# Performance work log

Measured on AMD Instinct MI355X. Metric: run time of the kernel, lower is better.

## Reference

```python
import jax, jax.numpy as jnp
import numpy as np

N_NODES = 200000
N_GRAPHS = 4000


def _sage_conv(x, src, dst, W_l, b_l, W_r, num_nodes):
    # PyG SAGEConv (aggr='mean'): out = lin_l(mean_{j in N(i)} x_j) + lin_r(x_i)
    msg_sum = jax.ops.segment_sum(x[src], dst, num_segments=num_nodes)      # [N, d]
    deg = jax.ops.segment_sum(jnp.ones_like(src, dtype=x.dtype), dst,
                              num_segments=num_nodes)                       # [N]
    mean_nbr = msg_sum / jnp.maximum(deg, 1.0)[:, None]
    return mean_nbr @ W_l.T + b_l + x @ W_r.T


def setup_inputs() -> dict:
    key = jax.random.key(0)
    ks = jax.random.split(key, 10)
    in_ch, hid, out = 32, 64, 2
    E = 3200000
    x = jax.random.normal(ks[0], (N_NODES, in_ch), dtype=jnp.float32)
    edge_index = jax.random.randint(ks[1], (2, E), 0, N_NODES, dtype=jnp.int64)
    batch = jnp.sort(jax.random.randint(ks[2], (N_NODES,), 0, N_GRAPHS, dtype=jnp.int64))

    def glorot(k, shape):
        lim = 1.0 / np.sqrt(shape[1])
        return jax.random.uniform(k, shape, jnp.float32, -lim, lim)

    return {
        "x": x,
        "edge_index": edge_index,
        "batch": batch,
        "W1_l": glorot(ks[3], (hid, in_ch)),
        "b1": jnp.zeros((hid,), jnp.float32),
        "W1_r": glorot(ks[4], (hid, in_ch)),
        "W2_l": glorot(ks[5], (hid, hid)),
        "b2": jnp.zeros((hid,), jnp.float32),
        "W2_r": glorot(ks[6], (hid, hid)),
        "W_lin": glorot(ks[7], (out, hid)),
        "b_lin": jnp.zeros((out,), jnp.float32),
    }


def reference(x, edge_index, batch, W1_l, b1, W1_r, W2_l, b2, W2_r, W_lin, b_lin):
    src, dst = edge_index[0], edge_index[1]
    h = jax.nn.relu(_sage_conv(x, src, dst, W1_l, b1, W1_r, N_NODES))
    h = jax.nn.relu(_sage_conv(h, src, dst, W2_l, b2, W2_r, N_NODES))
    # global_mean_pool over graph ids
    pool_sum = jax.ops.segment_sum(h, batch, num_segments=N_GRAPHS)          # [G, 64]
    cnt = jax.ops.segment_sum(jnp.ones_like(batch, dtype=h.dtype), batch,
                              num_segments=N_GRAPHS)                          # [G]
    pooled = pool_sum / jnp.maximum(cnt, 1.0)[:, None]
    return pooled @ W_lin.T + b_lin
```

## Files before the change

kernel.cpp:

```cpp
#include <hip/hip_runtime.h>
#include <hip/hip_bf16.h>


#define WS_ALIGN 64
#define EPB 4096
#define BSHIFT 8
#define BNODES 256
#define BCAP 6144
#define MAXNB 1024

typedef short bf16x8 __attribute__((ext_vector_type(8)));
typedef float f32x4 __attribute__((ext_vector_type(4)));

__device__ inline unsigned short f2bf(float f) {
    unsigned u = __float_as_uint(f);
    return (unsigned short)((u + 0x7fffu + ((u >> 16) & 1u)) >> 16);
}

__device__ inline void acc8(const uint4 u, float* a) {
    a[0] += __uint_as_float(u.x << 16);
    a[1] += __uint_as_float(u.x & 0xffff0000u);
    a[2] += __uint_as_float(u.y << 16);
    a[3] += __uint_as_float(u.y & 0xffff0000u);
    a[4] += __uint_as_float(u.z << 16);
    a[5] += __uint_as_float(u.z & 0xffff0000u);
    a[6] += __uint_as_float(u.w << 16);
    a[7] += __uint_as_float(u.w & 0xffff0000u);
}


__global__ void prep_kernel(const float* __restrict__ x, unsigned short* __restrict__ xb,
                            const float* __restrict__ W1_l, const float* __restrict__ W1_r,
                            const float* __restrict__ W2_l, const float* __restrict__ W2_r,
                            unsigned short* __restrict__ whi1, unsigned short* __restrict__ whi2,
                            int* __restrict__ bucketCursor, float* __restrict__ pool,
                            int N, int NB, int G, int total4) {
    const int gid = blockIdx.x * blockDim.x + threadIdx.x;
    if (gid < total4) {
        const float4 v = reinterpret_cast<const float4*>(x)[gid];
        ushort4 o;
        o.x = f2bf(v.x); o.y = f2bf(v.y); o.z = f2bf(v.z); o.w = f2bf(v.w);
        reinterpret_cast<ushort4*>(xb)[gid] = o;
    }
    if (gid < NB) bucketCursor[gid] = gid * BCAP;
    if (gid < G * 64) pool[gid] = 0.0f;
    if (gid < 64 * 64) {
        const int o = gid >> 6, k = gid & 63;
        const float v = (k < 32) ? W1_l[o * 32 + k] : W1_r[o * 32 + (k - 32)];
        whi1[gid] = f2bf(v);
    }
    if (gid < 64 * 128) {
        const int o = gid >> 7, k = gid & 127;
        const float v = (k < 64) ? W2_l[o * 64 + k] : W2_r[o * 64 + (k - 64)];
        whi2[gid] = f2bf(v);
    }
}


__global__ __launch_bounds__(256) void bucket_scatter_kernel(const int* __restrict__ src,
                                                             const int* __restrict__ dst,
                                                             int* __restrict__ bucketCursor,
                                                             unsigned* __restrict__ bucketData,
                                                             int E, int NB) {
    __shared__ int hist[MAXNB];
    __shared__ int cur[MAXNB];
    const int t = threadIdx.x;
    for (int i = t; i < MAXNB; i += 256) hist[i] = 0;
    __syncthreads();
    const int eBase = blockIdx.x * EPB + t;
    int s[16], b[16], dl[16];
#pragma unroll
    for (int j = 0; j < 16; ++j) {
        int e = eBase + j * 256;
        if (e < E) {
            int d = dst[e];
            s[j]  = src[e];
            b[j]  = d >> BSHIFT;
            dl[j] = d & (BNODES - 1);
            atomicAdd(&hist[b[j]], 1);
        } else {
            b[j] = -1;
        }
    }
    __syncthreads();
    for (int bb = t; bb < NB; bb += 256)
        if (hist[bb] > 0) cur[bb] = atomicAdd(&bucketCursor[bb], hist[bb]);
    __syncthreads();
#pragma unroll
    for (int j = 0; j < 16; ++j) {
        if (b[j] >= 0) {
            int pos = atomicAdd(&cur[b[j]], 1);
            if (pos < (b[j] + 1) * BCAP)
                bucketData[pos] = ((unsigned)s[j] << BSHIFT) | (unsigned)dl[j];
        }
    }
}

__global__ __launch_bounds__(256) void csr_build_kernel(const unsigned* __restrict__ bucketData,
                                                        const int* __restrict__ bucketCursor,
                                                        int* __restrict__ offs,
                                                        int* __restrict__ offe,
                                                        int* __restrict__ csr_src,
                                                        int N) {
    __shared__ int cnt[BNODES];
    __shared__ int sscan[BNODES];
    __shared__ int cur[BNODES];
    const int t   = threadIdx.x;
    const int bkt = blockIdx.x;
    const int nodeBase = bkt << BSHIFT;
    const int regionBase = bkt * BCAP;
    const int count = min(bucketCursor[bkt] - regionBase, BCAP);
    cnt[t] = 0;
    __syncthreads();
    for (int k = regionBase + t; k < regionBase + count; k += 256)
        atomicAdd(&cnt[bucketData[k] & (BNODES - 1)], 1);
    __syncthreads();
    int v0 = cnt[t];
    sscan[t] = v0;
    __syncthreads();
    for (int off = 1; off < 256; off <<= 1) {
        int v = (t >= off) ? sscan[t - off] : 0;
        __syncthreads();
        sscan[t] += v;
        __syncthreads();
    }
    const int excl = sscan[t] - v0;
    cur[t] = excl;
    const int node = nodeBase + t;
    if (node < N) {
        offs[node] = regionBase + excl;
        offe[node] = regionBase + excl + v0;
    }
    __syncthreads();
    for (int k = regionBase + t; k < regionBase + count; k += 256) {
        const unsigned v = bucketData[k];
        const int d = (int)(v & (BNODES - 1));
        const int pos = regionBase + atomicAdd(&cur[d], 1);
        csr_src[pos] = (int)(v >> BSHIFT);
    }
}


template <int DIN>
__launch_bounds__(256)
__global__ void fused_l1_kernel(const unsigned short* __restrict__ featb,
                                const unsigned short* __restrict__ whi,
                                const float* __restrict__ bias,
                                const int* __restrict__ csr_src,
                                const int* __restrict__ offs,
                                const int* __restrict__ offe,
                                unsigned short* __restrict__ houtb,
                                int N, int nSteps) {
    constexpr int K   = 2 * DIN;
    constexpr int STR = K + 8;
    constexpr int D8  = DIN / 8;
    __shared__ unsigned short A_s[64 * STR];
    const int tid  = threadIdx.x;
    const int lane = tid & 63;
    const int wave = tid >> 6;
    const int nodeBase = blockIdx.x * 64;
    const int rowBase  = wave * 16;

    for (int i = lane; i < 16 * D8; i += 64) {
        const int row = rowBase + i / D8, q = i % D8;
        const int n = min(nodeBase + row, N - 1);
        const uint4 u = *reinterpret_cast<const uint4*>(featb + (size_t)n * DIN + q * 8);
        *reinterpret_cast<uint4*>(&A_s[row * STR + DIN + q * 8]) = u;
    }
    {
        const int part = lane % D8;
        const int row  = rowBase + lane / D8;
        const int n = nodeBase + row;
        const uint4* base = reinterpret_cast<const uint4*>(featb);
        unsigned short* dp = &A_s[row * STR + part * 8];
        if (n < N) {
            const int beg = offs[n];
            const int end = offe[n];
            float a[8] = {0.f, 0.f, 0.f, 0.f, 0.f, 0.f, 0.f, 0.f};
            int k = beg;
            for (; k + 8 <= end; k += 8) {
                int s[8];
#pragma unroll
                for (int j = 0; j < 8; ++j) s[j] = csr_src[k + j];
                uint4 u[8];
#pragma unroll
                for (int j = 0; j < 8; ++j) u[j] = base[(size_t)s[j] * D8 + part];
#pragma unroll
                for (int j = 0; j < 8; ++j) acc8(u[j], a);
            }
            for (; k + 4 <= end; k += 4) {
                const int s0 = csr_src[k + 0];
                const int s1 = csr_src[k + 1];
                const int s2 = csr_src[k + 2];
                const int s3 = csr_src[k + 3];
                const uint4 u0 = base[(size_t)s0 * D8 + part];
                const uint4 u1 = base[(size_t)s1 * D8 + part];
                const uint4 u2 = base[(size_t)s2 * D8 + part];
                const uint4 u3 = base[(size_t)s3 * D8 + part];
                acc8(u0, a); acc8(u1, a); acc8(u2, a); acc8(u3, a);
            }
            for (; k < end; ++k) {
                const uint4 u = base[(size_t)csr_src[k] * D8 + part];
                acc8(u, a);
            }
            const float inv = 1.0f / fmaxf((float)(end - beg), 1.0f);
            ushort4 lo4, hi4;
            lo4.x = f2bf(a[0] * inv); lo4.y = f2bf(a[1] * inv);
            lo4.z = f2bf(a[2] * inv); lo4.w = f2bf(a[3] * inv);
            hi4.x = f2bf(a[4] * inv); hi4.y = f2bf(a[5] * inv);
            hi4.z = f2bf(a[6] * inv); hi4.w = f2bf(a[7] * inv);
            *reinterpret_cast<ushort4*>(dp)     = lo4;
            *reinterpret_cast<ushort4*>(dp + 4) = hi4;
        } else {
            const ushort4 z = {0, 0, 0, 0};
            *reinterpret_cast<ushort4*>(dp)     = z;
            *reinterpret_cast<ushort4*>(dp + 4) = z;
        }
    }

    asm volatile("s_waitcnt lgkmcnt(0)" ::: "memory");
    __builtin_amdgcn_sched_barrier(0);

    const int lr = lane & 15;
    const int q  = lane >> 4;
    f32x4 acc[4];
#pragma unroll
    for (int t = 0; t < 4; ++t) {
        const float b = bias[t * 16 + lr];
        acc[t] = (f32x4){b, b, b, b};
    }
    const unsigned short* Arow = &A_s[(rowBase + lr) * STR + q * 8];
    const unsigned short* Brow = whi + (size_t)lr * K + q * 8;
    for (int s = 0; s < nSteps; ++s) {
        const bf16x8 af = *reinterpret_cast<const bf16x8*>(Arow + s * 32);
#pragma unroll
        for (int t = 0; t < 4; ++t) {
            const bf16x8 bh = *reinterpret_cast<const bf16x8*>(
                Brow + (size_t)t * 16 * K + s * 32);
            acc[t] = __builtin_amdgcn_mfma_f32_16x16x32_bf16(af, bh, acc[t], 0, 0, 0);
        }
    }
    for (int reg = 0; reg < 4; ++reg) {
        const int n = nodeBase + rowBase + q * 4 + reg;
        if (n >= N) break;
#pragma unroll
        for (int t = 0; t < 4; ++t)
            houtb[(size_t)n * 64 + t * 16 + lr] = f2bf(fmaxf(acc[t][reg], 0.0f));
    }
}


__launch_bounds__(512)
__global__ void fused_l2_pool_kernel(const unsigned short* __restrict__ featb,
                                     const unsigned short* __restrict__ whi,
                                     const float* __restrict__ bias,
                                     const int* __restrict__ csr_src,
                                     const int* __restrict__ offs,
                                     const int* __restrict__ offe,
                                     const int* __restrict__ batch,
                                     float* __restrict__ pool_sum,
                                     int N, int nSteps) {
    constexpr int DIN = 64;
    constexpr int K   = 2 * DIN;
    constexpr int STR = K + 8;
    constexpr int D8  = DIN / 8;
    __shared__ unsigned short A_s[64 * STR];
    __shared__ float poolLds[16 * 65];
    const int tid  = threadIdx.x;
    const int lane = tid & 63;
    const int wave = tid >> 6;
    const int nodeBase = blockIdx.x * 64;

    for (int i = tid; i < 16 * 65; i += 512) poolLds[i] = 0.0f;

    {
        const int row = tid >> 3, q = tid & 7;
        const int n = min(nodeBase + row, N - 1);
        const uint4 u = *reinterpret_cast<const uint4*>(featb + (size_t)n * DIN + q * 8);
        *reinterpret_cast<uint4*>(&A_s[row * STR + DIN + q * 8]) = u;
    }

    {
        const int row  = tid >> 3;
        const int part = tid & 7;
        const int n = nodeBase + row;
        const uint4* base = reinterpret_cast<const uint4*>(featb);
        unsigned short* dp = &A_s[row * STR + part * 8];
        if (n < N) {
            const int beg = offs[n];
            const int end = offe[n];
            float a[8] = {0.f, 0.f, 0.f, 0.f, 0.f, 0.f, 0.f, 0.f};
            int k = beg;
            for (; k + 8 <= end; k += 8) {
                int s[8];
#pragma unroll
                for (int j = 0; j < 8; ++j) s[j] = csr_src[k + j];
                uint4 u[8];
#pragma unroll
                for (int j = 0; j < 8; ++j) u[j] = base[(size_t)s[j] * D8 + part];
#pragma unroll
                for (int j = 0; j < 8; ++j) acc8(u[j], a);
            }
            for (; k + 4 <= end; k += 4) {
                const int s0 = csr_src[k + 0];
                const int s1 = csr_src[k + 1];
                const int s2 = csr_src[k + 2];
                const int s3 = csr_src[k + 3];
                const uint4 u0 = base[(size_t)s0 * D8 + part];
                const uint4 u1 = base[(size_t)s1 * D8 + part];
                const uint4 u2 = base[(size_t)s2 * D8 + part];
                const uint4 u3 = base[(size_t)s3 * D8 + part];
                acc8(u0, a); acc8(u1, a); acc8(u2, a); acc8(u3, a);
            }
            for (; k < end; ++k) {
                const uint4 u = base[(size_t)csr_src[k] * D8 + part];
                acc8(u, a);
            }
            const float inv = 1.0f / fmaxf((float)(end - beg), 1.0f);
            ushort4 lo4, hi4;
            lo4.x = f2bf(a[0] * inv); lo4.y = f2bf(a[1] * inv);
            lo4.z = f2bf(a[2] * inv); lo4.w = f2bf(a[3] * inv);
            hi4.x = f2bf(a[4] * inv); hi4.y = f2bf(a[5] * inv);
            hi4.z = f2bf(a[6] * inv); hi4.w = f2bf(a[7] * inv);
            *reinterpret_cast<ushort4*>(dp)     = lo4;
            *reinterpret_cast<ushort4*>(dp + 4) = hi4;
        } else {
            const ushort4 z = {0, 0, 0, 0};
            *reinterpret_cast<ushort4*>(dp)     = z;
            *reinterpret_cast<ushort4*>(dp + 4) = z;
        }
    }
    __syncthreads();

    const int tg      = wave >> 1;
    const int colHalf = wave & 1;
    const int rowBase = tg * 16;
    const int lr = lane & 15;
    const int q  = lane >> 4;
    f32x4 acc[2];
#pragma unroll
    for (int tt = 0; tt < 2; ++tt) {
        const float b = bias[(colHalf * 2 + tt) * 16 + lr];
        acc[tt] = (f32x4){b, b, b, b};
    }
    const unsigned short* Arow = &A_s[(rowBase + lr) * STR + q * 8];
    const unsigned short* Brow = whi + (size_t)lr * K + q * 8;
    for (int s = 0; s < nSteps; ++s) {
        const bf16x8 af = *reinterpret_cast<const bf16x8*>(Arow + s * 32);
#pragma unroll
        for (int tt = 0; tt < 2; ++tt) {
            const bf16x8 bh = *reinterpret_cast<const bf16x8*>(
                Brow + (size_t)(colHalf * 2 + tt) * 16 * K + s * 32);
            acc[tt] = __builtin_amdgcn_mfma_f32_16x16x32_bf16(af, bh, acc[tt], 0, 0, 0);
        }
    }

    {
        const int g0 = batch[nodeBase];
        float ag[2] = {0.f, 0.f};
        int gcur = -1;
        auto flush_run = [&](int g) {
            const int r = g - g0;
            if (r < 16) {
#pragma unroll
                for (int tt = 0; tt < 2; ++tt)
                    atomicAdd(&poolLds[r * 65 + (colHalf * 2 + tt) * 16 + lr], ag[tt]);
            } else {
#pragma unroll
                for (int tt = 0; tt < 2; ++tt)
                    atomicAdd(&pool_sum[(size_t)g * 64 + (colHalf * 2 + tt) * 16 + lr],
                              ag[tt]);
            }
        };
        for (int reg = 0; reg < 4; ++reg) {
            const int n = nodeBase + rowBase + q * 4 + reg;
            if (n >= N) break;
            const int g = batch[n];
            if (g != gcur) {
                if (gcur >= 0) flush_run(gcur);
                gcur = g;
                ag[0] = ag[1] = 0.f;
            }
#pragma unroll
            for (int tt = 0; tt < 2; ++tt)
                ag[tt] += fmaxf(acc[tt][reg], 0.0f);
        }
        if (gcur >= 0) flush_run(gcur);
        __syncthreads();
        const int glast = batch[min(nodeBase + 63, N - 1)];
        const int S = min(glast - g0 + 1, 16);
        for (int i = tid; i < S * 64; i += 512) {
            const int r = i >> 6, c = i & 63;
            const float v = poolLds[r * 65 + c];
            float* dstp = &pool_sum[(size_t)(g0 + r) * 64 + c];
            if (r == 0 || r == S - 1) atomicAdd(dstp, v);
            else *dstp = v;
        }
    }
}


__device__ inline int lower_bound_batch(const int* __restrict__ batch, int N, int key) {
    int lo = 0, hi = N;
    while (lo < hi) {
        const int mid = (lo + hi) >> 1;
        if (batch[mid] < key) lo = mid + 1; else hi = mid;
    }
    return lo;
}

__global__ void final_kernel(const float* __restrict__ pool_sum,
                             const int* __restrict__ batch,
                             const float* __restrict__ W_lin,
                             const float* __restrict__ b_lin,
                             float* __restrict__ out, int G, int N) {
    int t = blockIdx.x * blockDim.x + threadIdx.x;
    if (t >= G * 2) return;
    int g = t >> 1, o = t & 1;
    const int c0 = lower_bound_batch(batch, N, g);
    const int c1 = lower_bound_batch(batch, N, g + 1);
    float inv = 1.0f / fmaxf((float)(c1 - c0), 1.0f);
    float acc = b_lin[o];
#pragma unroll
    for (int c = 0; c < 64; ++c)
        acc = fmaf(pool_sum[(size_t)g * 64 + c] * inv, W_lin[o * 64 + c], acc);
    out[t] = acc;
}

extern "C" void kernel_launch(void* const* d_in, const int* in_sizes, int n_in,
                              void* d_out, int out_size, void* d_ws, size_t ws_size,
                              hipStream_t stream) {
    const float* x     = (const float*)d_in[0];
    const int*   ei    = (const int*)d_in[1];
    const int*   batch = (const int*)d_in[2];
    const float* W1_l  = (const float*)d_in[3];
    const float* b1    = (const float*)d_in[4];
    const float* W1_r  = (const float*)d_in[5];
    const float* W2_l  = (const float*)d_in[6];
    const float* b2    = (const float*)d_in[7];
    const float* W2_r  = (const float*)d_in[8];
    const float* W_lin = (const float*)d_in[9];
    const float* b_lin = (const float*)d_in[10];

    const int N = in_sizes[0] / 32;
    const int E = in_sizes[1] / 2;
    const int G = out_size / 2;
    const int* src = ei;
    const int* dst = ei + E;
    const int NB = (N + BNODES - 1) >> BSHIFT;

    char* p = (char*)d_ws;
    auto carve = [&](size_t bytes) -> void* {
        void* r = (void*)p;
        p += (bytes + (WS_ALIGN - 1)) / WS_ALIGN * WS_ALIGN;
        return r;
    };
    int*            bucketCursor = (int*)carve((size_t)MAXNB * 4);
    unsigned*       bucketData   = (unsigned*)carve((size_t)NB * BCAP * 4);
    int*            offs         = (int*)carve((size_t)N * 4);
    int*            offe         = (int*)carve((size_t)N * 4);
    int*            csr_src      = (int*)carve((size_t)NB * BCAP * 4);
    unsigned short* xb           = (unsigned short*)carve((size_t)N * 32 * 2);
    unsigned short* h1b          = (unsigned short*)carve((size_t)N * 64 * 2);
    unsigned short* whi1         = (unsigned short*)carve(64 * 64 * 2);
    unsigned short* whi2         = (unsigned short*)carve(64 * 128 * 2);
    float*          pool         = (float*)carve((size_t)G * 64 * 4);
    float*          out          = (float*)d_out;

    const int TB = 256;
    const int total4 = N * 32 / 4;
    prep_kernel<<<(total4 + TB - 1) / TB, TB, 0, stream>>>(
        x, xb, W1_l, W1_r, W2_l, W2_r, whi1, whi2, bucketCursor, pool,
        N, NB, G, total4);
    bucket_scatter_kernel<<<(E + EPB - 1) / EPB, TB, 0, stream>>>(src, dst, bucketCursor,
                                                                  bucketData, E, NB);
    csr_build_kernel<<<NB, TB, 0, stream>>>(bucketData, bucketCursor, offs, offe, csr_src, N);

    fused_l1_kernel<32><<<(N + 63) / 64, TB, 0, stream>>>(
        xb, whi1, b1, csr_src, offs, offe, h1b, N, 2);

    fused_l2_pool_kernel<<<(N + 63) / 64, 512, 0, stream>>>(
        h1b, whi2, b2, csr_src, offs, offe, batch, pool, N, 4);

    final_kernel<<<(G * 2 + TB - 1) / TB, TB, 0, stream>>>(pool, batch, W_lin, b_lin,
                                                           out, G, N);
}
```

Baseline: 353.2 us.

## Stage bucket scatter and CSR build in LDS, make GNN layers persistent

The bucket scatter now sorts each block's edges locally in shared memory through a prefix scan and writes them out contiguously per bucket, which should coalesce global writes. CSR build copies each bucket into LDS, permutes it there, and writes csr_src with coalesced stores. Both layer kernels become grid-stride persistent loops with capped grids, and layer 2 drops from 512 to 256 threads per block, with each wave handling 16 rows in two passes. This cuts launch and tail overhead but lowers per-block parallelism in the gather phase and raises LDS use per block.

```diff
diff --git a/kernel.cpp b/kernel.cpp
--- a/kernel.cpp
+++ b/kernel.cpp
@@ -57,51 +57,81 @@
 }
 
 
-__global__ __launch_bounds__(256) void bucket_scatter_kernel(const int* __restrict__ src,
+__global__ __launch_bounds__(512) void bucket_scatter_kernel(const int* __restrict__ src,
                                                              const int* __restrict__ dst,
                                                              int* __restrict__ bucketCursor,
                                                              unsigned* __restrict__ bucketData,
                                                              int E, int NB) {
     __shared__ int hist[MAXNB];
-    __shared__ int cur[MAXNB];
+    __shared__ int lofs[MAXNB];
+    __shared__ int lcur[MAXNB];
+    __shared__ int gbase[MAXNB];
+    __shared__ int sscan[512];
+    __shared__ unsigned staged[EPB];
+    __shared__ int gaddr[EPB];
     const int t = threadIdx.x;
-    for (int i = t; i < MAXNB; i += 256) hist[i] = 0;
+    for (int i = t; i < MAXNB; i += 512) hist[i] = 0;
     __syncthreads();
     const int eBase = blockIdx.x * EPB + t;
-    int s[16], b[16], dl[16];
-#pragma unroll
-    for (int j = 0; j < 16; ++j) {
-        int e = eBase + j * 256;
+    int bkt[8]; unsigned rec[8];
+#pragma unroll
+    for (int j = 0; j < 8; ++j) {
+        const int e = eBase + j * 512;
         if (e < E) {
-            int d = dst[e];
-            s[j]  = src[e];
-            b[j]  = d >> BSHIFT;
-            dl[j] = d & (BNODES - 1);
-            atomicAdd(&hist[b[j]], 1);
+            const int d = dst[e];
+            bkt[j] = d >> BSHIFT;
+            rec[j] = ((unsigned)src[e] << BSHIFT) | (unsigned)(d & (BNODES - 1));
+            atomicAdd(&hist[bkt[j]], 1);
         } else {
-            b[j] = -1;
-        }
-    }
-    __syncthreads();
-    for (int bb = t; bb < NB; bb += 256)
-        if (hist[bb] > 0) cur[bb] = atomicAdd(&bucketCursor[bb], hist[bb]);
-    __syncthreads();
-#pragma unroll
-    for (int j = 0; j < 16; ++j) {
-        if (b[j] >= 0) {
-            int pos = atomicAdd(&cur[b[j]], 1);
-            if (pos < (b[j] + 1) * BCAP)
-                bucketData[pos] = ((unsigned)s[j] << BSHIFT) | (unsigned)dl[j];
-        }
-    }
-}
-
-__global__ __launch_bounds__(256) void csr_build_kernel(const unsigned* __restrict__ bucketData,
+            bkt[j] = -1;
+        }
+    }
+    __syncthreads();
+    const int b2 = t * 2;
+    const int h0 = hist[b2], h1 = hist[b2 + 1];
+    const int tsum = h0 + h1;
+    sscan[t] = tsum;
+    __syncthreads();
+    for (int off = 1; off < 512; off <<= 1) {
+        const int v = (t >= off) ? sscan[t - off] : 0;
+        __syncthreads();
+        sscan[t] += v;
+        __syncthreads();
+    }
+    const int excl = sscan[t] - tsum;
+    lofs[b2]     = excl;
+    lofs[b2 + 1] = excl + h0;
+    lcur[b2]     = excl;
+    lcur[b2 + 1] = excl + h0;
+    for (int bb = t; bb < NB; bb += 512)
+        if (hist[bb] > 0) gbase[bb] = atomicAdd(&bucketCursor[bb], hist[bb]);
+    __syncthreads();
+#pragma unroll
+    for (int j = 0; j < 8; ++j) {
+        if (bkt[j] >= 0) {
+            const int b = bkt[j];
+            const int lp = atomicAdd(&lcur[b], 1);
+            staged[lp] = rec[j];
+            const int gp = gbase[b] + (lp - lofs[b]);
+            gaddr[lp] = (gp < (b + 1) * BCAP) ? gp : -1;
+        }
+    }
+    __syncthreads();
+    const int cnt = min(EPB, E - blockIdx.x * EPB);
+    for (int i = t; i < cnt; i += 512) {
+        const int p = gaddr[i];
+        if (p >= 0) bucketData[p] = staged[i];
+    }
+}
+
+__global__ __launch_bounds__(512) void csr_build_kernel(const unsigned* __restrict__ bucketData,
                                                         const int* __restrict__ bucketCursor,
                                                         int* __restrict__ offs,
                                                         int* __restrict__ offe,
                                                         int* __restrict__ csr_src,
                                                         int N) {
+    __shared__ unsigned ldsIn[BCAP];
+    __shared__ unsigned ldsOut[BCAP];
     __shared__ int cnt[BNODES];
     __shared__ int sscan[BNODES];
     __shared__ int cur[BNODES];
@@ -110,34 +140,42 @@
     const int nodeBase = bkt << BSHIFT;
     const int regionBase = bkt * BCAP;
     const int count = min(bucketCursor[bkt] - regionBase, BCAP);
-    cnt[t] = 0;
-    __syncthreads();
-    for (int k = regionBase + t; k < regionBase + count; k += 256)
-        atomicAdd(&cnt[bucketData[k] & (BNODES - 1)], 1);
-    __syncthreads();
-    int v0 = cnt[t];
-    sscan[t] = v0;
-    __syncthreads();
-    for (int off = 1; off < 256; off <<= 1) {
-        int v = (t >= off) ? sscan[t - off] : 0;
+    if (t < BNODES) cnt[t] = 0;
+    __syncthreads();
+    for (int k = t; k < count; k += 512) {
+        const unsigned v = bucketData[regionBase + k];
+        ldsIn[k] = v;
+        atomicAdd(&cnt[v & (BNODES - 1)], 1);
+    }
+    __syncthreads();
+    int v0 = 0;
+    if (t < BNODES) { v0 = cnt[t]; sscan[t] = v0; }
+    __syncthreads();
+    for (int off = 1; off < BNODES; off <<= 1) {
+        int v = 0;
+        if (t < BNODES && t >= off) v = sscan[t - off];
         __syncthreads();
-        sscan[t] += v;
+        if (t < BNODES) sscan[t] += v;
         __syncthreads();
     }
-    const int excl = sscan[t] - v0;
-    cur[t] = excl;
-    const int node = nodeBase + t;
-    if (node < N) {
-        offs[node] = regionBase + excl;
-        offe[node] = regionBase + excl + v0;
-    }
-    __syncthreads();
-    for (int k = regionBase + t; k < regionBase + count; k += 256) {
-        const unsigned v = bucketData[k];
-        const int d = (int)(v & (BNODES - 1));
-        const int pos = regionBase + atomicAdd(&cur[d], 1);
-        csr_src[pos] = (int)(v >> BSHIFT);
-    }
+    if (t < BNODES) {
+        const int excl = sscan[t] - v0;
+        cur[t] = excl;
+        const int node = nodeBase + t;
+        if (node < N) {
+            offs[node] = regionBase + excl;
+            offe[node] = regionBase + excl + v0;
+        }
+    }
+    __syncthreads();
+    for (int k = t; k < count; k += 512) {
+        const unsigned v = ldsIn[k];
+        const int p = atomicAdd(&cur[v & (BNODES - 1)], 1);
+        ldsOut[p] = v >> BSHIFT;
+    }
+    __syncthreads();
+    for (int k = t; k < count; k += 512)
+        csr_src[regionBase + k] = (int)ldsOut[k];
 }
 
 
@@ -158,99 +196,104 @@
     const int tid  = threadIdx.x;
     const int lane = tid & 63;
     const int wave = tid >> 6;
-    const int nodeBase = blockIdx.x * 64;
-    const int rowBase  = wave * 16;
-
-    for (int i = lane; i < 16 * D8; i += 64) {
-        const int row = rowBase + i / D8, q = i % D8;
-        const int n = min(nodeBase + row, N - 1);
-        const uint4 u = *reinterpret_cast<const uint4*>(featb + (size_t)n * DIN + q * 8);
-        *reinterpret_cast<uint4*>(&A_s[row * STR + DIN + q * 8]) = u;
-    }
-    {
-        const int part = lane % D8;
-        const int row  = rowBase + lane / D8;
-        const int n = nodeBase + row;
-        const uint4* base = reinterpret_cast<const uint4*>(featb);
-        unsigned short* dp = &A_s[row * STR + part * 8];
-        if (n < N) {
-            const int beg = offs[n];
-            const int end = offe[n];
-            float a[8] = {0.f, 0.f, 0.f, 0.f, 0.f, 0.f, 0.f, 0.f};
-            int k = beg;
-            for (; k + 8 <= end; k += 8) {
-                int s[8];
-#pragma unroll
-                for (int j = 0; j < 8; ++j) s[j] = csr_src[k + j];
-                uint4 u[8];
-#pragma unroll
-                for (int j = 0; j < 8; ++j) u[j] = base[(size_t)s[j] * D8 + part];
-#pragma unroll
-                for (int j = 0; j < 8; ++j) acc8(u[j], a);
-            }
-            for (; k + 4 <= end; k += 4) {
-                const int s0 = csr_src[k + 0];
-                const int s1 = csr_src[k + 1];
-                const int s2 = csr_src[k + 2];
-                const int s3 = csr_src[k + 3];
-                const uint4 u0 = base[(size_t)s0 * D8 + part];
-                const uint4 u1 = base[(size_t)s1 * D8 + part];
-                const uint4 u2 = base[(size_t)s2 * D8 + part];
-                const uint4 u3 = base[(size_t)s3 * D8 + part];
-                acc8(u0, a); acc8(u1, a); acc8(u2, a); acc8(u3, a);
-            }
-            for (; k < end; ++k) {
-                const uint4 u = base[(size_t)csr_src[k] * D8 + part];
-                acc8(u, a);
-            }
-            const float inv = 1.0f / fmaxf((float)(end - beg), 1.0f);
-            ushort4 lo4, hi4;
-            lo4.x = f2bf(a[0] * inv); lo4.y = f2bf(a[1] * inv);
-            lo4.z = f2bf(a[2] * inv); lo4.w = f2bf(a[3] * inv);
-            hi4.x = f2bf(a[4] * inv); hi4.y = f2bf(a[5] * inv);
-            hi4.z = f2bf(a[6] * inv); hi4.w = f2bf(a[7] * inv);
-            *reinterpret_cast<ushort4*>(dp)     = lo4;
-            *reinterpret_cast<ushort4*>(dp + 4) = hi4;
-        } else {
-            const ushort4 z = {0, 0, 0, 0};
-            *reinterpret_cast<ushort4*>(dp)     = z;
-            *reinterpret_cast<ushort4*>(dp + 4) = z;
-        }
-    }
-
-    asm volatile("s_waitcnt lgkmcnt(0)" ::: "memory");
-    __builtin_amdgcn_sched_barrier(0);
-
+    const int rowBase = wave * 16;
     const int lr = lane & 15;
     const int q  = lane >> 4;
-    f32x4 acc[4];
-#pragma unroll
-    for (int t = 0; t < 4; ++t) {
-        const float b = bias[t * 16 + lr];
-        acc[t] = (f32x4){b, b, b, b};
-    }
-    const unsigned short* Arow = &A_s[(rowBase + lr) * STR + q * 8];
-    const unsigned short* Brow = whi + (size_t)lr * K + q * 8;
-    for (int s = 0; s < nSteps; ++s) {
-        const bf16x8 af = *reinterpret_cast<const bf16x8*>(Arow + s * 32);
-#pragma unroll
-        for (int t = 0; t < 4; ++t) {
-            const bf16x8 bh = *reinterpret_cast<const bf16x8*>(
-                Brow + (size_t)t * 16 * K + s * 32);
-            acc[t] = __builtin_amdgcn_mfma_f32_16x16x32_bf16(af, bh, acc[t], 0, 0, 0);
-        }
-    }
-    for (int reg = 0; reg < 4; ++reg) {
-        const int n = nodeBase + rowBase + q * 4 + reg;
-        if (n >= N) break;
-#pragma unroll
-        for (int t = 0; t < 4; ++t)
-            houtb[(size_t)n * 64 + t * 16 + lr] = f2bf(fmaxf(acc[t][reg], 0.0f));
-    }
-}
-
-
-__launch_bounds__(512)
+    const int nWT = (N + 15) >> 4;
+    const int wstride = gridDim.x * 4;
+
+    for (int wt = blockIdx.x * 4 + wave; wt < nWT; wt += wstride) {
+        const int nodeBase = wt * 16;
+
+        for (int i = lane; i < 16 * D8; i += 64) {
+            const int row = i / D8, qq = i % D8;
+            const int n = min(nodeBase + row, N - 1);
+            const uint4 u = *reinterpret_cast<const uint4*>(featb + (size_t)n * DIN + qq * 8);
+            *reinterpret_cast<uint4*>(&A_s[(rowBase + row) * STR + DIN + qq * 8]) = u;
+        }
+        {
+            const int part = lane % D8;
+            const int row  = lane / D8;
+            const int n = nodeBase + row;
+            const uint4* base = reinterpret_cast<const uint4*>(featb);
+            unsigned short* dp = &A_s[(rowBase + row) * STR + part * 8];
+            if (n < N) {
+                const int beg = offs[n];
+                const int end = offe[n];
+                float a[8] = {0.f, 0.f, 0.f, 0.f, 0.f, 0.f, 0.f, 0.f};
+                int k = beg;
+                for (; k + 8 <= end; k += 8) {
+                    int s[8];
+#pragma unroll
+                    for (int j = 0; j < 8; ++j) s[j] = csr_src[k + j];
+                    uint4 u[8];
+#pragma unroll
+                    for (int j = 0; j < 8; ++j) u[j] = base[(size_t)s[j] * D8 + part];
+#pragma unroll
+                    for (int j = 0; j < 8; ++j) acc8(u[j], a);
+                }
+                for (; k + 4 <= end; k += 4) {
+                    const int s0 = csr_src[k + 0];
+                    const int s1 = csr_src[k + 1];
+                    const int s2 = csr_src[k + 2];
+                    const int s3 = csr_src[k + 3];
+                    const uint4 u0 = base[(size_t)s0 * D8 + part];
+                    const uint4 u1 = base[(size_t)s1 * D8 + part];
+                    const uint4 u2 = base[(size_t)s2 * D8 + part];
+                    const uint4 u3 = base[(size_t)s3 * D8 + part];
+                    acc8(u0, a); acc8(u1, a); acc8(u2, a); acc8(u3, a);
+                }
+                for (; k < end; ++k) {
+                    const uint4 u = base[(size_t)csr_src[k] * D8 + part];
+                    acc8(u, a);
+                }
+                const float inv = 1.0f / fmaxf((float)(end - beg), 1.0f);
+                ushort4 lo4, hi4;
+                lo4.x = f2bf(a[0] * inv); lo4.y = f2bf(a[1] * inv);
+                lo4.z = f2bf(a[2] * inv); lo4.w = f2bf(a[3] * inv);
+                hi4.x = f2bf(a[4] * inv); hi4.y = f2bf(a[5] * inv);
+                hi4.z = f2bf(a[6] * inv); hi4.w = f2bf(a[7] * inv);
+                *reinterpret_cast<ushort4*>(dp)     = lo4;
+                *reinterpret_cast<ushort4*>(dp + 4) = hi4;
+            } else {
+                const ushort4 z = {0, 0, 0, 0};
+                *reinterpret_cast<ushort4*>(dp)     = z;
+                *reinterpret_cast<ushort4*>(dp + 4) = z;
+            }
+        }
+
+        asm volatile("s_waitcnt lgkmcnt(0)" ::: "memory");
+        __builtin_amdgcn_sched_barrier(0);
+
+        f32x4 acc[4];
+#pragma unroll
+        for (int t4 = 0; t4 < 4; ++t4) {
+            const float b = bias[t4 * 16 + lr];
+            acc[t4] = (f32x4){b, b, b, b};
+        }
+        const unsigned short* Arow = &A_s[(rowBase + lr) * STR + q * 8];
+        const unsigned short* Brow = whi + (size_t)lr * K + q * 8;
+        for (int s = 0; s < nSteps; ++s) {
+            const bf16x8 af = *reinterpret_cast<const bf16x8*>(Arow + s * 32);
+#pragma unroll
+            for (int t4 = 0; t4 < 4; ++t4) {
+                const bf16x8 bh = *reinterpret_cast<const bf16x8*>(
+                    Brow + (size_t)t4 * 16 * K + s * 32);
+                acc[t4] = __builtin_amdgcn_mfma_f32_16x16x32_bf16(af, bh, acc[t4], 0, 0, 0);
+            }
+        }
+        for (int reg = 0; reg < 4; ++reg) {
+            const int n = nodeBase + q * 4 + reg;
+            if (n >= N) break;
+#pragma unroll
+            for (int t4 = 0; t4 < 4; ++t4)
+                houtb[(size_t)n * 64 + t4 * 16 + lr] = f2bf(fmaxf(acc[t4][reg], 0.0f));
+        }
+    }
+}
+
+
+__launch_bounds__(256)
 __global__ void fused_l2_pool_kernel(const unsigned short* __restrict__ featb,
                                      const unsigned short* __restrict__ whi,
                                      const float* __restrict__ bias,
@@ -260,141 +303,150 @@
                                      const int* __restrict__ batch,
                                      float* __restrict__ pool_sum,
                                      int N, int nSteps) {
-    constexpr int DIN = 64;
-    constexpr int K   = 2 * DIN;
-    constexpr int STR = K + 8;
-    constexpr int D8  = DIN / 8;
+    constexpr int DIN   = 64;
+    constexpr int K     = 2 * DIN;
+    constexpr int STR   = K + 8;
+    constexpr int D8    = DIN / 8;
+    constexpr int NPW   = 64 / D8;
+    constexpr int NPASS = 16 / NPW;
     __shared__ unsigned short A_s[64 * STR];
     __shared__ float poolLds[16 * 65];
     const int tid  = threadIdx.x;
     const int lane = tid & 63;
     const int wave = tid >> 6;
-    const int nodeBase = blockIdx.x * 64;
-
-    for (int i = tid; i < 16 * 65; i += 512) poolLds[i] = 0.0f;
-
-    {
-        const int row = tid >> 3, q = tid & 7;
-        const int n = min(nodeBase + row, N - 1);
-        const uint4 u = *reinterpret_cast<const uint4*>(featb + (size_t)n * DIN + q * 8);
-        *reinterpret_cast<uint4*>(&A_s[row * STR + DIN + q * 8]) = u;
-    }
-
-    {
-        const int row  = tid >> 3;
-        const int part = tid & 7;
-        const int n = nodeBase + row;
-        const uint4* base = reinterpret_cast<const uint4*>(featb);
-        unsigned short* dp = &A_s[row * STR + part * 8];
-        if (n < N) {
-            const int beg = offs[n];
-            const int end = offe[n];
-            float a[8] = {0.f, 0.f, 0.f, 0.f, 0.f, 0.f, 0.f, 0.f};
-            int k = beg;
-            for (; k + 8 <= end; k += 8) {
-                int s[8];
-#pragma unroll
-                for (int j = 0; j < 8; ++j) s[j] = csr_src[k + j];
-                uint4 u[8];
-#pragma unroll
-                for (int j = 0; j < 8; ++j) u[j] = base[(size_t)s[j] * D8 + part];
-#pragma unroll
-                for (int j = 0; j < 8; ++j) acc8(u[j], a);
-            }
-            for (; k + 4 <= end; k += 4) {
-                const int s0 = csr_src[k + 0];
-                const int s1 = csr_src[k + 1];
-                const int s2 = csr_src[k + 2];
-                const int s3 = csr_src[k + 3];
-                const uint4 u0 = base[(size_t)s0 * D8 + part];
-                const uint4 u1 = base[(size_t)s1 * D8 + part];
-                const uint4 u2 = base[(size_t)s2 * D8 + part];
-                const uint4 u3 = base[(size_t)s3 * D8 + part];
-                acc8(u0, a); acc8(u1, a); acc8(u2, a); acc8(u3, a);
-            }
-            for (; k < end; ++k) {
-                const uint4 u = base[(size_t)csr_src[k] * D8 + part];
-                acc8(u, a);
-            }
-            const float inv = 1.0f / fmaxf((float)(end - beg), 1.0f);
-            ushort4 lo4, hi4;
-            lo4.x = f2bf(a[0] * inv); lo4.y = f2bf(a[1] * inv);
-            lo4.z = f2bf(a[2] * inv); lo4.w = f2bf(a[3] * inv);
-            hi4.x = f2bf(a[4] * inv); hi4.y = f2bf(a[5] * inv);
-            hi4.z = f2bf(a[6] * inv); hi4.w = f2bf(a[7] * inv);
-            *reinterpret_cast<ushort4*>(dp)     = lo4;
-            *reinterpret_cast<ushort4*>(dp + 4) = hi4;
-        } else {
-            const ushort4 z = {0, 0, 0, 0};
-            *reinterpret_cast<ushort4*>(dp)     = z;
-            *reinterpret_cast<ushort4*>(dp + 4) = z;
-        }
-    }
-    __syncthreads();
-
-    const int tg      = wave >> 1;
-    const int colHalf = wave & 1;
-    const int rowBase = tg * 16;
+    const int rowBase = wave * 16;
     const int lr = lane & 15;
     const int q  = lane >> 4;
-    f32x4 acc[2];
-#pragma unroll
-    for (int tt = 0; tt < 2; ++tt) {
-        const float b = bias[(colHalf * 2 + tt) * 16 + lr];
-        acc[tt] = (f32x4){b, b, b, b};
-    }
-    const unsigned short* Arow = &A_s[(rowBase + lr) * STR + q * 8];
-    const unsigned short* Brow = whi + (size_t)lr * K + q * 8;
-    for (int s = 0; s < nSteps; ++s) {
-        const bf16x8 af = *reinterpret_cast<const bf16x8*>(Arow + s * 32);
-#pragma unroll
-        for (int tt = 0; tt < 2; ++tt) {
-            const bf16x8 bh = *reinterpret_cast<const bf16x8*>(
-                Brow + (size_t)(colHalf * 2 + tt) * 16 * K + s * 32);
-            acc[tt] = __builtin_amdgcn_mfma_f32_16x16x32_bf16(af, bh, acc[tt], 0, 0, 0);
-        }
-    }
-
-    {
-        const int g0 = batch[nodeBase];
-        float ag[2] = {0.f, 0.f};
-        int gcur = -1;
-        auto flush_run = [&](int g) {
-            const int r = g - g0;
-            if (r < 16) {
-#pragma unroll
-                for (int tt = 0; tt < 2; ++tt)
-                    atomicAdd(&poolLds[r * 65 + (colHalf * 2 + tt) * 16 + lr], ag[tt]);
-            } else {
-#pragma unroll
-                for (int tt = 0; tt < 2; ++tt)
-                    atomicAdd(&pool_sum[(size_t)g * 64 + (colHalf * 2 + tt) * 16 + lr],
-                              ag[tt]);
+    const int nTiles = (N + 63) >> 6;
+
+    for (int tile = blockIdx.x; tile < nTiles; tile += gridDim.x) {
+        const int nodeBase = tile * 64;
+
+        for (int i = tid; i < 16 * 65; i += 256) poolLds[i] = 0.0f;
+        __syncthreads();
+
+        for (int i = lane; i < 16 * D8; i += 64) {
+            const int row = i / D8, qq = i % D8;
+            const int n = min(nodeBase + rowBase + row, N - 1);
+            const uint4 u = *reinterpret_cast<const uint4*>(featb + (size_t)n * DIN + qq * 8);
+            *reinterpret_cast<uint4*>(&A_s[(rowBase + row) * STR + DIN + qq * 8]) = u;
+        }
+        {
+            const int part = lane % D8;
+            const uint4* base = reinterpret_cast<const uint4*>(featb);
+#pragma unroll
+            for (int pass = 0; pass < NPASS; ++pass) {
+                const int row = rowBase + pass * NPW + lane / D8;
+                const int n = nodeBase + row;
+                unsigned short* dp = &A_s[row * STR + part * 8];
+                if (n < N) {
+                    const int beg = offs[n];
+                    const int end = offe[n];
+                    float a[8] = {0.f, 0.f, 0.f, 0.f, 0.f, 0.f, 0.f, 0.f};
+                    int k = beg;
+                    for (; k + 8 <= end; k += 8) {
+                        int s[8];
+#pragma unroll
+                        for (int j = 0; j < 8; ++j) s[j] = csr_src[k + j];
+                        uint4 u[8];
+#pragma unroll
+                        for (int j = 0; j < 8; ++j) u[j] = base[(size_t)s[j] * D8 + part];
+#pragma unroll
+                        for (int j = 0; j < 8; ++j) acc8(u[j], a);
+                    }
+                    for (; k + 4 <= end; k += 4) {
+                        const int s0 = csr_src[k + 0];
+                        const int s1 = csr_src[k + 1];
+                        const int s2 = csr_src[k + 2];
+                        const int s3 = csr_src[k + 3];
+                        const uint4 u0 = base[(size_t)s0 * D8 + part];
+                        const uint4 u1 = base[(size_t)s1 * D8 + part];
+                        const uint4 u2 = base[(size_t)s2 * D8 + part];
+                        const uint4 u3 = base[(size_t)s3 * D8 + part];
+                        acc8(u0, a); acc8(u1, a); acc8(u2, a); acc8(u3, a);
+                    }
+                    for (; k < end; ++k) {
+                        const uint4 u = base[(size_t)csr_src[k] * D8 + part];
+                        acc8(u, a);
+                    }
+                    const float inv = 1.0f / fmaxf((float)(end - beg), 1.0f);
+                    ushort4 lo4, hi4;
+                    lo4.x = f2bf(a[0] * inv); lo4.y = f2bf(a[1] * inv);
+                    lo4.z = f2bf(a[2] * inv); lo4.w = f2bf(a[3] * inv);
+                    hi4.x = f2bf(a[4] * inv); hi4.y = f2bf(a[5] * inv);
+                    hi4.z = f2bf(a[6] * inv); hi4.w = f2bf(a[7] * inv);
+                    *reinterpret_cast<ushort4*>(dp)     = lo4;
+                    *reinterpret_cast<ushort4*>(dp + 4) = hi4;
+                } else {
+                    const ushort4 z = {0, 0, 0, 0};
+                    *reinterpret_cast<ushort4*>(dp)     = z;
+                    *reinterpret_cast<ushort4*>(dp + 4) = z;
+                }
             }
-        };
-        for (int reg = 0; reg < 4; ++reg) {
-            const int n = nodeBase + rowBase + q * 4 + reg;
-            if (n >= N) break;
-            const int g = batch[n];
-            if (g != gcur) {
-                if (gcur >= 0) flush_run(gcur);
-                gcur = g;
-                ag[0] = ag[1] = 0.f;
+        }
+
+        asm volatile("s_waitcnt lgkmcnt(0)" ::: "memory");
+        __builtin_amdgcn_sched_barrier(0);
+
+        f32x4 acc[4];
+#pragma unroll
+        for (int t4 = 0; t4 < 4; ++t4) {
+            const float b = bias[t4 * 16 + lr];
+            acc[t4] = (f32x4){b, b, b, b};
+        }
+        const unsigned short* Arow = &A_s[(rowBase + lr) * STR + q * 8];
+        const unsigned short* Brow = whi + (size_t)lr * K + q * 8;
+        for (int s = 0; s < nSteps; ++s) {
+            const bf16x8 af = *reinterpret_cast<const bf16x8*>(Arow + s * 32);
+#pragma unroll
+            for (int t4 = 0; t4 < 4; ++t4) {
+                const bf16x8 bh = *reinterpret_cast<const bf16x8*>(
+                    Brow + (size_t)t4 * 16 * K + s * 32);
+                acc[t4] = __builtin_amdgcn_mfma_f32_16x16x32_bf16(af, bh, acc[t4], 0, 0, 0);
             }
-#pragma unroll
-            for (int tt = 0; tt < 2; ++tt)
-                ag[tt] += fmaxf(acc[tt][reg], 0.0f);
-        }
-        if (gcur >= 0) flush_run(gcur);
-        __syncthreads();
-        const int glast = batch[min(nodeBase + 63, N - 1)];
-        const int S = min(glast - g0 + 1, 16);
-        for (int i = tid; i < S * 64; i += 512) {
-            const int r = i >> 6, c = i & 63;
-            const float v = poolLds[r * 65 + c];
-            float* dstp = &pool_sum[(size_t)(g0 + r) * 64 + c];
-            if (r == 0 || r == S - 1) atomicAdd(dstp, v);
-            else *dstp = v;
+        }
+
+        {
+            const int g0 = batch[nodeBase];
+            float ag[4] = {0.f, 0.f, 0.f, 0.f};
+            int gcur = -1;
+            auto flush_run = [&](int g) {
+                const int r = g - g0;
+                if (r < 16) {
+#pragma unroll
+                    for (int t4 = 0; t4 < 4; ++t4)
+                        atomicAdd(&poolLds[r * 65 + t4 * 16 + lr], ag[t4]);
+                } else {
+#pragma unroll
+                    for (int t4 = 0; t4 < 4; ++t4)
+                        atomicAdd(&pool_sum[(size_t)g * 64 + t4 * 16 + lr], ag[t4]);
+                }
+            };
+            for (int reg = 0; reg < 4; ++reg) {
+                const int n = nodeBase + rowBase + q * 4 + reg;
+                if (n >= N) break;
+                const int g = batch[n];
+                if (g != gcur) {
+                    if (gcur >= 0) flush_run(gcur);
+                    gcur = g;
+                    ag[0] = ag[1] = ag[2] = ag[3] = 0.f;
+                }
+#pragma unroll
+                for (int t4 = 0; t4 < 4; ++t4)
+                    ag[t4] += fmaxf(acc[t4][reg], 0.0f);
+            }
+            if (gcur >= 0) flush_run(gcur);
+            __syncthreads();
+            const int glast = batch[min(nodeBase + 63, N - 1)];
+            const int S = min(glast - g0 + 1, 16);
+            for (int i = tid; i < S * 64; i += 256) {
+                const int r = i >> 6, c = i & 63;
+                const float v = poolLds[r * 65 + c];
+                float* dstp = &pool_sum[(size_t)(g0 + r) * 64 + c];
+                if (r == 0 || r == S - 1) atomicAdd(dstp, v);
+                else *dstp = v;
+            }
+            __syncthreads();
         }
     }
 }
@@ -472,14 +524,18 @@
     prep_kernel<<<(total4 + TB - 1) / TB, TB, 0, stream>>>(
         x, xb, W1_l, W1_r, W2_l, W2_r, whi1, whi2, bucketCursor, pool,
         N, NB, G, total4);
-    bucket_scatter_kernel<<<(E + EPB - 1) / EPB, TB, 0, stream>>>(src, dst, bucketCursor,
-                                                                  bucketData, E, NB);
-    csr_build_kernel<<<NB, TB, 0, stream>>>(bucketData, bucketCursor, offs, offe, csr_src, N);
-
-    fused_l1_kernel<32><<<(N + 63) / 64, TB, 0, stream>>>(
+    bucket_scatter_kernel<<<(E + EPB - 1) / EPB, 512, 0, stream>>>(src, dst, bucketCursor,
+                                                                   bucketData, E, NB);
+    csr_build_kernel<<<NB, 512, 0, stream>>>(bucketData, bucketCursor, offs, offe, csr_src, N);
+
+    const int nWT = (N + 15) >> 4;
+    const int grid1 = min(2048, (nWT + 3) / 4);
+    fused_l1_kernel<32><<<grid1, TB, 0, stream>>>(
         xb, whi1, b1, csr_src, offs, offe, h1b, N, 2);
 
-    fused_l2_pool_kernel<<<(N + 63) / 64, 512, 0, stream>>>(
+    const int nTiles = (N + 63) >> 6;
+    const int grid2 = min(1792, nTiles);
+    fused_l2_pool_kernel<<<grid2, TB, 0, stream>>>(
         h1b, whi2, b2, csr_src, offs, offe, batch, pool, N, 4);
 
     final_kernel<<<(G * 2 + TB - 1) / TB, TB, 0, stream>>>(pool, batch, W_lin, b_lin,
```

New measurement: 323.6 us. 8.4% less time.
